# Kernel optimization log

Measured on AMD Instinct MI355X. Metric: run time of the kernel, lower is better.

The kernel has to match this reference:

```python
import jax, jax.numpy as jnp
import numpy as np

B, C, H, W = 8, 256, 56, 56
CI = 64  # inter_channels = C // reduction


def setup_inputs() -> dict:
    key = jax.random.key(0)
    ks = jax.random.split(key, 8)
    s = 0.05
    return {
        "x": jax.random.normal(ks[0], (B, C, H, W), jnp.float32),
        "Wq": jax.random.normal(ks[1], (CI, C), jnp.float32) * s,
        "bq": jax.random.normal(ks[2], (CI,), jnp.float32) * s,
        "Wk": jax.random.normal(ks[3], (CI, C), jnp.float32) * s,
        "bk": jax.random.normal(ks[4], (CI,), jnp.float32) * s,
        "Wv": jax.random.normal(ks[5], (C, C), jnp.float32) * s,
        "bv": jax.random.normal(ks[6], (C,), jnp.float32) * s,
        "gamma": jax.random.normal(ks[7], (1,), jnp.float32) * s,
    }


def reference(x, Wq, bq, Wk, bk, Wv, bv, gamma):
    b, c, h, w = x.shape
    n = h * w
    xf = x.reshape(b, c, n)  # [B, C, N]
    # 1x1 convs == per-pixel linear projections
    q = jnp.einsum('oc,bcn->bno', Wq, xf) + bq          # [B, N, CI]
    k = jnp.einsum('oc,bcn->bon', Wk, xf) + bk[:, None]  # [B, CI, N]
    score = jnp.einsum('bno,bom->bnm', q, k)             # [B, N, N] (no scaling, as in source)
    attention = jax.nn.softmax(score, axis=-1)
    v = jnp.einsum('oc,bcn->bon', Wv, xf) + bv[:, None]  # [B, C, N]
    # out[b,c,i] = sum_j v[b,c,j] * attention[b,i,j]  (== bmm(V, att^T))
    out = jnp.einsum('bcj,bij->bci', v, attention).reshape(b, c, h, w)
    return gamma[0] * out + x
```

## Files before the change

kernel.cpp:

```cpp
#include <hip/hip_runtime.h>


constexpr int B_  = 8;
constexpr int C_  = 256;
constexpr int CI_ = 64;
constexpr int N_  = 3136;
constexpr int JS  = 4;
constexpr int JT  = 32;
constexpr int VSP = 40;
constexpr int PN  = 64;
constexpr int XSP = C_ + 8;

typedef __attribute__((ext_vector_type(8))) short short8;
typedef __attribute__((ext_vector_type(4))) float f32x4;

static __device__ inline ushort f2b(float f) {
    unsigned u = __float_as_uint(f);
    return (ushort)((u + 0x7fffu + ((u >> 16) & 1u)) >> 16);
}
static __device__ inline float b2f(ushort h) {
    return __uint_as_float(((unsigned)h) << 16);
}

__global__ __launch_bounds__(256)
void pre_kernel(const float* __restrict__ x,
                const float* __restrict__ Wq, const float* __restrict__ Wk,
                const float* __restrict__ Wv,
                ushort* __restrict__ xT, ushort* __restrict__ wqk, ushort* __restrict__ wv)
{
    __shared__ float ts[64][65];
    const int bx  = blockIdx.x;
    const int tid = threadIdx.x;

    if (bx >= B_ * 196) {
        int i = (bx - B_ * 196) * 256 + tid;
        if (i < 16384)      wqk[i] = f2b(Wq[i]);
        else if (i < 32768) wqk[i] = f2b(Wk[i - 16384]);
        wv[i] = f2b(Wv[i]);
        return;
    }

    const int b  = bx / 196;
    const int rm = bx % 196;
    const int n0 = (rm >> 2) * 64;
    const int c0 = (rm & 3) * 64;

    const float* src = x + ((size_t)b * C_ + c0) * N_ + n0;
    #pragma unroll
    for (int rep = 0; rep < 16; rep++) {
        int e = rep * 256 + tid;
        int c = e >> 6, n = e & 63;
        ts[c][n] = src[(size_t)c * N_ + n];
    }
    __syncthreads();
    ushort* dst = xT + ((size_t)b * N_ + n0) * C_ + c0;
    #pragma unroll
    for (int rep = 0; rep < 8; rep++) {
        int e = rep * 256 + tid;
        int n = e >> 5, c2 = (e & 31) * 2;
        ushort2 o;
        o.x = f2b(ts[c2][n]);
        o.y = f2b(ts[c2 + 1][n]);
        *(ushort2*)(dst + (size_t)n * C_ + c2) = o;
    }
}

__global__ __launch_bounds__(256)
void proj_kernel(const ushort* __restrict__ xT, const ushort* __restrict__ wqk,
                 const ushort* __restrict__ wv,
                 const float* __restrict__ bq, const float* __restrict__ bk,
                 const float* __restrict__ bv,
                 ushort* __restrict__ qb, ushort* __restrict__ kb, ushort* __restrict__ vt)
{
    __shared__ ushort xs[PN][XSP];
    const int b   = blockIdx.x / 49;
    const int n0  = (blockIdx.x % 49) * PN;
    const int tid = threadIdx.x;
    const int w    = tid >> 6;
    const int lane = tid & 63;
    const int m16  = lane & 15;
    const int quad = lane >> 4;

    {
        const ushort* src = xT + ((size_t)b * N_ + n0) * C_;
        #pragma unroll
        for (int rep = 0; rep < 8; rep++) {
            int e = rep * 256 + tid;
            int row = e >> 5, ch = (e & 31) * 8;
            *(short8*)&xs[row][ch] = *(const short8*)(src + (size_t)row * C_ + ch);
        }
    }
    __syncthreads();

    {
        f32x4 acc[2][4];
        #pragma unroll
        for (int mt = 0; mt < 2; mt++)
            #pragma unroll
            for (int nt = 0; nt < 4; nt++) acc[mt][nt] = (f32x4){0.f, 0.f, 0.f, 0.f};

        #pragma unroll
        for (int kk = 0; kk < 8; kk++) {
            short8 af[2];
            #pragma unroll
            for (int mt = 0; mt < 2; mt++)
                af[mt] = *(const short8*)(wqk + (size_t)(w * 32 + mt * 16 + m16) * C_ + kk * 32 + quad * 8);
            #pragma unroll
            for (int nt = 0; nt < 4; nt++) {
                short8 bf = *(const short8*)&xs[nt * 16 + m16][kk * 32 + quad * 8];
                #pragma unroll
                for (int mt = 0; mt < 2; mt++)
                    acc[mt][nt] = __builtin_amdgcn_mfma_f32_16x16x32_bf16(af[mt], bf, acc[mt][nt], 0, 0, 0);
            }
        }
        const float* bias = (w < 2) ? bq : bk;
        ushort* dst = (w < 2) ? qb : kb;
        const int obase = (w & 1) * 32;
        #pragma unroll
        for (int mt = 0; mt < 2; mt++) {
            f32x4 bs = *(const f32x4*)(bias + obase + mt * 16 + quad * 4);
            #pragma unroll
            for (int nt = 0; nt < 4; nt++) {
                ushort4 pk;
                pk.x = f2b(acc[mt][nt][0] + bs[0]);
                pk.y = f2b(acc[mt][nt][1] + bs[1]);
                pk.z = f2b(acc[mt][nt][2] + bs[2]);
                pk.w = f2b(acc[mt][nt][3] + bs[3]);
                *(ushort4*)(dst + ((size_t)b * N_ + n0 + nt * 16 + m16) * CI_ + obase + mt * 16 + quad * 4) = pk;
            }
        }
    }

    {
        f32x4 vacc[4][4];
        #pragma unroll
        for (int mt = 0; mt < 4; mt++)
            #pragma unroll
            for (int nt = 0; nt < 4; nt++) vacc[mt][nt] = (f32x4){0.f, 0.f, 0.f, 0.f};

        #pragma unroll
        for (int kk = 0; kk < 8; kk++) {
            short8 af[4];
            #pragma unroll
            for (int mt = 0; mt < 4; mt++)
                af[mt] = *(const short8*)&xs[mt * 16 + m16][kk * 32 + quad * 8];
            #pragma unroll
            for (int nt = 0; nt < 4; nt++) {
                short8 bf = *(const short8*)(wv + (size_t)(w * 64 + nt * 16 + m16) * C_ + kk * 32 + quad * 8);
                #pragma unroll
                for (int mt = 0; mt < 4; mt++)
                    vacc[mt][nt] = __builtin_amdgcn_mfma_f32_16x16x32_bf16(af[mt], bf, vacc[mt][nt], 0, 0, 0);
            }
        }
        #pragma unroll
        for (int nt = 0; nt < 4; nt++) {
            int c = w * 64 + nt * 16 + m16;
            float bvc = bv[c];
            #pragma unroll
            for (int mt = 0; mt < 4; mt++) {
                ushort4 pk;
                pk.x = f2b(vacc[mt][nt][0] + bvc);
                pk.y = f2b(vacc[mt][nt][1] + bvc);
                pk.z = f2b(vacc[mt][nt][2] + bvc);
                pk.w = f2b(vacc[mt][nt][3] + bvc);
                *(ushort4*)(vt + ((size_t)b * C_ + c) * N_ + n0 + mt * 16 + quad * 4) = pk;
            }
        }
    }
}

__global__ __launch_bounds__(256, 5)
void attn_kernel(const ushort* __restrict__ qb, const ushort* __restrict__ kb,
                 const ushort* __restrict__ vt,
                 ushort* __restrict__ op, float* __restrict__ lp)
{
    __shared__ __align__(16) ushort vs[C_][VSP];

    const int bx   = blockIdx.x;
    const int js   = bx & (JS - 1);
    const int t    = (bx >> 2) % 98;
    const int b    = bx / (98 * JS);
    const int tid  = threadIdx.x;
    const int w    = tid >> 6;
    const int lane = tid & 63;
    const int m16  = lane & 15;
    const int quad = lane >> 4;
    const int i0   = t * 32 + (w & 1) * 16;
    const int ch0  = (w >> 1) * 128;

    const int steps = (js == 0) ? 13 : 12;
    const int jbase = ((js == 0) ? 0 : (1 + 12 * js)) * JT;

    const ushort* vtb = vt + (size_t)b * C_ * N_;
    const ushort* kbb = kb + (size_t)b * N_ * CI_;

    short8 qf[2];
    {
        const ushort* qbase = qb + ((size_t)b * N_ + i0 + m16) * CI_;
        qf[0] = *(const short8*)(qbase + quad * 8);
        qf[1] = *(const short8*)(qbase + 32 + quad * 8);
    }

    f32x4 O[8];
    #pragma unroll
    for (int ct = 0; ct < 8; ct++) O[ct] = (f32x4){0.f, 0.f, 0.f, 0.f};
    float lsum = 0.f;

    const int sc  = tid >> 2;
    const int seg = tid & 3;
    const int p0  = (seg & 1) * 16 + (seg >> 1) * 4;

    short8 pr[4];
    #define PREFETCH(J0)                                                       \
        {                                                                      \
            _Pragma("unroll")                                                  \
            for (int p = 0; p < 4; p++)                                        \
                pr[p] = *(const short8*)(vtb + (size_t)(p * 64 + sc) * N_ + (J0) + seg * 8); \
        }
    #define COMMIT()                                                           \
        {                                                                      \
            _Pragma("unroll")                                                  \
            for (int p = 0; p < 4; p++) {                                      \
                *(ushort4*)&vs[p * 64 + sc][p0]     = ((const ushort4*)&pr[p])[0]; \
                *(ushort4*)&vs[p * 64 + sc][p0 + 8] = ((const ushort4*)&pr[p])[1]; \
            }                                                                  \
        }

    PREFETCH(jbase)
    COMMIT()
    __syncthreads();

    for (int st = 0; st < steps; st++) {
        const int j0 = jbase + st * JT;
        if (st + 1 < steps) PREFETCH(j0 + JT)

        short8 pa;
        #pragma unroll
        for (int h = 0; h < 2; h++) {
            const ushort* krow = kbb + (size_t)(j0 + h * 16 + m16) * CI_;
            short8 kf0 = *(const short8*)(krow + quad * 8);
            short8 kf1 = *(const short8*)(krow + 32 + quad * 8);
            f32x4 T = (f32x4){0.f, 0.f, 0.f, 0.f};
            T = __builtin_amdgcn_mfma_f32_16x16x32_bf16(kf0, qf[0], T, 0, 0, 0);
            T = __builtin_amdgcn_mfma_f32_16x16x32_bf16(kf1, qf[1], T, 0, 0, 0);
            #pragma unroll
            for (int r = 0; r < 4; r++) {
                float pv = __expf(T[r] - 12.0f);
                lsum += pv;
                pa[h * 4 + r] = (short)f2b(pv);
            }
        }

        #pragma unroll
        for (int ct = 0; ct < 8; ct++) {
            short8 vf = *(const short8*)&vs[ch0 + ct * 16 + m16][quad * 8];
            O[ct] = __builtin_amdgcn_mfma_f32_16x16x32_bf16(pa, vf, O[ct], 0, 0, 0);
        }
        __syncthreads();
        if (st + 1 < steps) COMMIT()
        __syncthreads();
    }

    {
        float v = lsum;
        v += __shfl_xor(v, 16);
        v += __shfl_xor(v, 32);
        if (w < 2 && lane < 16)
            lp[(size_t)(b * JS + js) * N_ + i0 + lane] = v;
    }

    ushort* opb = op + (size_t)(b * JS + js) * C_ * N_;
    #pragma unroll
    for (int ct = 0; ct < 8; ct++) {
        ushort4 pk;
        pk.x = f2b(O[ct][0]);
        pk.y = f2b(O[ct][1]);
        pk.z = f2b(O[ct][2]);
        pk.w = f2b(O[ct][3]);
        *(ushort4*)(opb + (size_t)(ch0 + ct * 16 + m16) * N_ + i0 + quad * 4) = pk;
    }
    #undef PREFETCH
    #undef COMMIT
}

__global__ __launch_bounds__(256)
void reduce_kernel(const ushort* __restrict__ op, const float* __restrict__ lp,
                   const float* __restrict__ x, const float* __restrict__ gamma_p,
                   float* __restrict__ out)
{
    const int g  = blockIdx.x * 256 + threadIdx.x;
    const int i4 = g % (N_ / 4);
    const int c  = (g / (N_ / 4)) % C_;
    const int b  = g / ((N_ / 4) * C_);
    const size_t io = (size_t)i4 * 4;
    const float g0 = gamma_p[0];

    f32x4 acc = (f32x4){0.f, 0.f, 0.f, 0.f};
    f32x4 lt  = (f32x4){0.f, 0.f, 0.f, 0.f};
    #pragma unroll
    for (int js = 0; js < JS; js++) {
        ushort4 a = *(const ushort4*)(op + ((size_t)(b * JS + js) * C_ + c) * N_ + io);
        f32x4   l = *(const f32x4*)(lp + (size_t)(b * JS + js) * N_ + io);
        acc[0] += b2f(a.x); acc[1] += b2f(a.y); acc[2] += b2f(a.z); acc[3] += b2f(a.w);
        lt += l;
    }

    const size_t xo = ((size_t)b * C_ + c) * N_ + io;
    f32x4 xv = *(const f32x4*)(x + xo);
    f32x4 ov;
    #pragma unroll
    for (int u = 0; u < 4; u++) ov[u] = acc[u] * (g0 / lt[u]) + xv[u];
    *(f32x4*)(out + xo) = ov;
}

extern "C" void kernel_launch(void* const* d_in, const int* in_sizes, int n_in,
                              void* d_out, int out_size, void* d_ws, size_t ws_size,
                              hipStream_t stream)
{
    const float* x  = (const float*)d_in[0];
    const float* Wq = (const float*)d_in[1];
    const float* bq = (const float*)d_in[2];
    const float* Wk = (const float*)d_in[3];
    const float* bk = (const float*)d_in[4];
    const float* Wv = (const float*)d_in[5];
    const float* bv = (const float*)d_in[6];
    const float* gm = (const float*)d_in[7];
    float* out = (float*)d_out;

    ushort* qb   = (ushort*)d_ws;
    ushort* kb   = qb + (size_t)B_ * N_ * CI_;
    ushort* vt   = kb + (size_t)B_ * N_ * CI_;
    ushort* xT   = vt + (size_t)B_ * C_ * N_;
    ushort* wqk  = xT + (size_t)B_ * N_ * C_;
    ushort* wv   = wqk + 128 * C_;
    ushort* op   = wv + 256 * C_;
    float*  lpf  = (float*)(op + (size_t)B_ * JS * C_ * N_);

    hipLaunchKernelGGL(pre_kernel, dim3(B_ * 196 + 256), dim3(256), 0, stream,
                       x, Wq, Wk, Wv, xT, wqk, wv);
    hipLaunchKernelGGL(proj_kernel, dim3(B_ * 49), dim3(256), 0, stream,
                       xT, wqk, wv, bq, bk, bv, qb, kb, vt);
    hipLaunchKernelGGL(attn_kernel, dim3(B_ * 98 * JS), dim3(256), 0, stream,
                       qb, kb, vt, op, lpf);
    hipLaunchKernelGGL(reduce_kernel, dim3(B_ * C_ * (N_ / 4) / 256), dim3(256), 0, stream,
                       op, lpf, x, gm, out);
}
```

Before: 234.8 us.

## Double query rows per attention wave, double-buffer V tile, prefetch K, halve proj tile

Each attention wave now handles two 16-row query groups, so every K fragment and V tile in shared memory serves twice as many MFMAs. The grid is halved and each split covers about 25 key steps. The V staging tile is double-buffered, which removes one barrier per step, and K fragments are prefetched into registers one step ahead. The projection kernel tile drops from 64 to 32 pixels to double its block count. The cost is higher register use, with launch bounds lowered to 3 waves, and twice the LDS per block.

```diff
diff --git a/kernel.cpp b/kernel.cpp
--- a/kernel.cpp
+++ b/kernel.cpp
@@ -8,7 +8,7 @@
 constexpr int JS  = 4;
 constexpr int JT  = 32;
 constexpr int VSP = 40;
-constexpr int PN  = 64;
+constexpr int PN  = 32;
 constexpr int XSP = C_ + 8;
 
 typedef __attribute__((ext_vector_type(8))) short short8;
@@ -73,8 +73,8 @@
                  ushort* __restrict__ qb, ushort* __restrict__ kb, ushort* __restrict__ vt)
 {
     __shared__ ushort xs[PN][XSP];
-    const int b   = blockIdx.x / 49;
-    const int n0  = (blockIdx.x % 49) * PN;
+    const int b   = blockIdx.x / 98;
+    const int n0  = (blockIdx.x % 98) * PN;
     const int tid = threadIdx.x;
     const int w    = tid >> 6;
     const int lane = tid & 63;
@@ -84,7 +84,7 @@
     {
         const ushort* src = xT + ((size_t)b * N_ + n0) * C_;
         #pragma unroll
-        for (int rep = 0; rep < 8; rep++) {
+        for (int rep = 0; rep < 4; rep++) {
             int e = rep * 256 + tid;
             int row = e >> 5, ch = (e & 31) * 8;
             *(short8*)&xs[row][ch] = *(const short8*)(src + (size_t)row * C_ + ch);
@@ -93,11 +93,11 @@
     __syncthreads();
 
     {
-        f32x4 acc[2][4];
+        f32x4 acc[2][2];
         #pragma unroll
         for (int mt = 0; mt < 2; mt++)
             #pragma unroll
-            for (int nt = 0; nt < 4; nt++) acc[mt][nt] = (f32x4){0.f, 0.f, 0.f, 0.f};
+            for (int nt = 0; nt < 2; nt++) acc[mt][nt] = (f32x4){0.f, 0.f, 0.f, 0.f};
 
         #pragma unroll
         for (int kk = 0; kk < 8; kk++) {
@@ -106,7 +106,7 @@
             for (int mt = 0; mt < 2; mt++)
                 af[mt] = *(const short8*)(wqk + (size_t)(w * 32 + mt * 16 + m16) * C_ + kk * 32 + quad * 8);
             #pragma unroll
-            for (int nt = 0; nt < 4; nt++) {
+            for (int nt = 0; nt < 2; nt++) {
                 short8 bf = *(const short8*)&xs[nt * 16 + m16][kk * 32 + quad * 8];
                 #pragma unroll
                 for (int mt = 0; mt < 2; mt++)
@@ -120,7 +120,7 @@
         for (int mt = 0; mt < 2; mt++) {
             f32x4 bs = *(const f32x4*)(bias + obase + mt * 16 + quad * 4);
             #pragma unroll
-            for (int nt = 0; nt < 4; nt++) {
+            for (int nt = 0; nt < 2; nt++) {
                 ushort4 pk;
                 pk.x = f2b(acc[mt][nt][0] + bs[0]);
                 pk.y = f2b(acc[mt][nt][1] + bs[1]);
@@ -132,23 +132,23 @@
     }
 
     {
-        f32x4 vacc[4][4];
-        #pragma unroll
-        for (int mt = 0; mt < 4; mt++)
+        f32x4 vacc[2][4];
+        #pragma unroll
+        for (int mt = 0; mt < 2; mt++)
             #pragma unroll
             for (int nt = 0; nt < 4; nt++) vacc[mt][nt] = (f32x4){0.f, 0.f, 0.f, 0.f};
 
         #pragma unroll
         for (int kk = 0; kk < 8; kk++) {
-            short8 af[4];
-            #pragma unroll
-            for (int mt = 0; mt < 4; mt++)
+            short8 af[2];
+            #pragma unroll
+            for (int mt = 0; mt < 2; mt++)
                 af[mt] = *(const short8*)&xs[mt * 16 + m16][kk * 32 + quad * 8];
             #pragma unroll
             for (int nt = 0; nt < 4; nt++) {
                 short8 bf = *(const short8*)(wv + (size_t)(w * 64 + nt * 16 + m16) * C_ + kk * 32 + quad * 8);
                 #pragma unroll
-                for (int mt = 0; mt < 4; mt++)
+                for (int mt = 0; mt < 2; mt++)
                     vacc[mt][nt] = __builtin_amdgcn_mfma_f32_16x16x32_bf16(af[mt], bf, vacc[mt][nt], 0, 0, 0);
             }
         }
@@ -157,7 +157,7 @@
             int c = w * 64 + nt * 16 + m16;
             float bvc = bv[c];
             #pragma unroll
-            for (int mt = 0; mt < 4; mt++) {
+            for (int mt = 0; mt < 2; mt++) {
                 ushort4 pk;
                 pk.x = f2b(vacc[mt][nt][0] + bvc);
                 pk.y = f2b(vacc[mt][nt][1] + bvc);
@@ -169,118 +169,152 @@
     }
 }
 
-__global__ __launch_bounds__(256, 5)
+__global__ __launch_bounds__(256, 3)
 void attn_kernel(const ushort* __restrict__ qb, const ushort* __restrict__ kb,
                  const ushort* __restrict__ vt,
                  ushort* __restrict__ op, float* __restrict__ lp)
 {
-    __shared__ __align__(16) ushort vs[C_][VSP];
+    __shared__ __align__(16) ushort vs[2][C_][VSP];
 
     const int bx   = blockIdx.x;
     const int js   = bx & (JS - 1);
-    const int t    = (bx >> 2) % 98;
-    const int b    = bx / (98 * JS);
+    const int t    = (bx >> 2) % 49;
+    const int b    = bx / (49 * JS);
     const int tid  = threadIdx.x;
     const int w    = tid >> 6;
     const int lane = tid & 63;
     const int m16  = lane & 15;
     const int quad = lane >> 4;
-    const int i0   = t * 32 + (w & 1) * 16;
+    const int i0   = t * 64 + (w & 1) * 32;
     const int ch0  = (w >> 1) * 128;
 
-    const int steps = (js == 0) ? 13 : 12;
-    const int jbase = ((js == 0) ? 0 : (1 + 12 * js)) * JT;
+    const int steps = (js < 2) ? 25 : 24;
+    const int jbase = ((js < 2) ? js * 25 : 50 + (js - 2) * 24) * JT;
 
     const ushort* vtb = vt + (size_t)b * C_ * N_;
     const ushort* kbb = kb + (size_t)b * N_ * CI_;
 
-    short8 qf[2];
-    {
-        const ushort* qbase = qb + ((size_t)b * N_ + i0 + m16) * CI_;
-        qf[0] = *(const short8*)(qbase + quad * 8);
-        qf[1] = *(const short8*)(qbase + 32 + quad * 8);
-    }
-
-    f32x4 O[8];
-    #pragma unroll
-    for (int ct = 0; ct < 8; ct++) O[ct] = (f32x4){0.f, 0.f, 0.f, 0.f};
-    float lsum = 0.f;
-
-    const int sc  = tid >> 2;
-    const int seg = tid & 3;
-    const int p0  = (seg & 1) * 16 + (seg >> 1) * 4;
-
-    short8 pr[4];
-    #define PREFETCH(J0)                                                       \
-        {                                                                      \
-            _Pragma("unroll")                                                  \
-            for (int p = 0; p < 4; p++)                                        \
-                pr[p] = *(const short8*)(vtb + (size_t)(p * 64 + sc) * N_ + (J0) + seg * 8); \
-        }
-    #define COMMIT()                                                           \
-        {                                                                      \
-            _Pragma("unroll")                                                  \
-            for (int p = 0; p < 4; p++) {                                      \
-                *(ushort4*)&vs[p * 64 + sc][p0]     = ((const ushort4*)&pr[p])[0]; \
-                *(ushort4*)&vs[p * 64 + sc][p0 + 8] = ((const ushort4*)&pr[p])[1]; \
-            }                                                                  \
-        }
-
-    PREFETCH(jbase)
-    COMMIT()
+    short8 qf[2][2];
+    #pragma unroll
+    for (int qg = 0; qg < 2; qg++) {
+        const ushort* qbase = qb + ((size_t)b * N_ + i0 + qg * 16 + m16) * CI_;
+        qf[qg][0] = *(const short8*)(qbase + quad * 8);
+        qf[qg][1] = *(const short8*)(qbase + 32 + quad * 8);
+    }
+
+    f32x4 O[2][8];
+    #pragma unroll
+    for (int qg = 0; qg < 2; qg++)
+        #pragma unroll
+        for (int ct = 0; ct < 8; ct++) O[qg][ct] = (f32x4){0.f, 0.f, 0.f, 0.f};
+    float lsum[2] = {0.f, 0.f};
+
+    const int sc = tid >> 2;
+    const int s4 = (tid & 3) * 4;
+    const int sp = (tid & 3) * 8;
+
+    uint2 vr[4][2];
+    #define VLOAD(J0)                                                           \
+        {                                                                       \
+            _Pragma("unroll")                                                   \
+            for (int p = 0; p < 4; p++) {                                       \
+                const ushort* r = vtb + (size_t)(p * 64 + sc) * N_ + (J0);      \
+                vr[p][0] = *(const uint2*)(r + s4);                             \
+                vr[p][1] = *(const uint2*)(r + 16 + s4);                        \
+            }                                                                   \
+        }
+    #define VCOMMIT(BUF)                                                        \
+        {                                                                       \
+            _Pragma("unroll")                                                   \
+            for (int p = 0; p < 4; p++) {                                       \
+                uint4 t4;                                                       \
+                t4.x = vr[p][0].x; t4.y = vr[p][0].y;                           \
+                t4.z = vr[p][1].x; t4.w = vr[p][1].y;                           \
+                *(uint4*)&vs[BUF][p * 64 + sc][sp] = t4;                        \
+            }                                                                   \
+        }
+    #define KLOAD(DST, J0)                                                      \
+        {                                                                       \
+            _Pragma("unroll")                                                   \
+            for (int h = 0; h < 2; h++) {                                       \
+                const ushort* kr = kbb + (size_t)((J0) + h * 16 + m16) * CI_;   \
+                DST[h * 2 + 0] = *(const short8*)(kr + quad * 8);               \
+                DST[h * 2 + 1] = *(const short8*)(kr + 32 + quad * 8);          \
+            }                                                                   \
+        }
+
+    short8 kc[4];
+    KLOAD(kc, jbase)
+    VLOAD(jbase)
+    VCOMMIT(0)
     __syncthreads();
 
+    int buf = 0;
     for (int st = 0; st < steps; st++) {
         const int j0 = jbase + st * JT;
-        if (st + 1 < steps) PREFETCH(j0 + JT)
-
-        short8 pa;
+        const bool more = (st + 1 < steps);
+        short8 kn[4];
+        if (more) { VLOAD(j0 + JT) KLOAD(kn, j0 + JT) }
+
+        short8 pa[2];
         #pragma unroll
         for (int h = 0; h < 2; h++) {
-            const ushort* krow = kbb + (size_t)(j0 + h * 16 + m16) * CI_;
-            short8 kf0 = *(const short8*)(krow + quad * 8);
-            short8 kf1 = *(const short8*)(krow + 32 + quad * 8);
-            f32x4 T = (f32x4){0.f, 0.f, 0.f, 0.f};
-            T = __builtin_amdgcn_mfma_f32_16x16x32_bf16(kf0, qf[0], T, 0, 0, 0);
-            T = __builtin_amdgcn_mfma_f32_16x16x32_bf16(kf1, qf[1], T, 0, 0, 0);
+            f32x4 T0 = (f32x4){0.f, 0.f, 0.f, 0.f};
+            f32x4 T1 = (f32x4){0.f, 0.f, 0.f, 0.f};
+            T0 = __builtin_amdgcn_mfma_f32_16x16x32_bf16(kc[h * 2 + 0], qf[0][0], T0, 0, 0, 0);
+            T1 = __builtin_amdgcn_mfma_f32_16x16x32_bf16(kc[h * 2 + 0], qf[1][0], T1, 0, 0, 0);
+            T0 = __builtin_amdgcn_mfma_f32_16x16x32_bf16(kc[h * 2 + 1], qf[0][1], T0, 0, 0, 0);
+            T1 = __builtin_amdgcn_mfma_f32_16x16x32_bf16(kc[h * 2 + 1], qf[1][1], T1, 0, 0, 0);
             #pragma unroll
             for (int r = 0; r < 4; r++) {
-                float pv = __expf(T[r] - 12.0f);
-                lsum += pv;
-                pa[h * 4 + r] = (short)f2b(pv);
+                float p0 = __expf(T0[r] - 12.0f);
+                float p1 = __expf(T1[r] - 12.0f);
+                lsum[0] += p0;
+                lsum[1] += p1;
+                pa[0][h * 4 + r] = (short)f2b(p0);
+                pa[1][h * 4 + r] = (short)f2b(p1);
             }
         }
 
         #pragma unroll
         for (int ct = 0; ct < 8; ct++) {
-            short8 vf = *(const short8*)&vs[ch0 + ct * 16 + m16][quad * 8];
-            O[ct] = __builtin_amdgcn_mfma_f32_16x16x32_bf16(pa, vf, O[ct], 0, 0, 0);
-        }
+            short8 vf = *(const short8*)&vs[buf][ch0 + ct * 16 + m16][quad * 8];
+            O[0][ct] = __builtin_amdgcn_mfma_f32_16x16x32_bf16(pa[0], vf, O[0][ct], 0, 0, 0);
+            O[1][ct] = __builtin_amdgcn_mfma_f32_16x16x32_bf16(pa[1], vf, O[1][ct], 0, 0, 0);
+        }
+
+        if (more) VCOMMIT(buf ^ 1)
         __syncthreads();
-        if (st + 1 < steps) COMMIT()
-        __syncthreads();
-    }
-
-    {
-        float v = lsum;
+        if (more) {
+            kc[0] = kn[0]; kc[1] = kn[1]; kc[2] = kn[2]; kc[3] = kn[3];
+        }
+        buf ^= 1;
+    }
+    #undef VLOAD
+    #undef VCOMMIT
+    #undef KLOAD
+
+    #pragma unroll
+    for (int qg = 0; qg < 2; qg++) {
+        float v = lsum[qg];
         v += __shfl_xor(v, 16);
         v += __shfl_xor(v, 32);
-        if (w < 2 && lane < 16)
-            lp[(size_t)(b * JS + js) * N_ + i0 + lane] = v;
+        if ((w >> 1) == 0 && lane < 16)
+            lp[(size_t)(b * JS + js) * N_ + i0 + qg * 16 + lane] = v;
     }
 
     ushort* opb = op + (size_t)(b * JS + js) * C_ * N_;
     #pragma unroll
-    for (int ct = 0; ct < 8; ct++) {
-        ushort4 pk;
-        pk.x = f2b(O[ct][0]);
-        pk.y = f2b(O[ct][1]);
-        pk.z = f2b(O[ct][2]);
-        pk.w = f2b(O[ct][3]);
-        *(ushort4*)(opb + (size_t)(ch0 + ct * 16 + m16) * N_ + i0 + quad * 4) = pk;
-    }
-    #undef PREFETCH
-    #undef COMMIT
+    for (int qg = 0; qg < 2; qg++)
+        #pragma unroll
+        for (int ct = 0; ct < 8; ct++) {
+            ushort4 pk;
+            pk.x = f2b(O[qg][ct][0]);
+            pk.y = f2b(O[qg][ct][1]);
+            pk.z = f2b(O[qg][ct][2]);
+            pk.w = f2b(O[qg][ct][3]);
+            *(ushort4*)(opb + (size_t)(ch0 + ct * 16 + m16) * N_ + i0 + qg * 16 + quad * 4) = pk;
+        }
 }
 
 __global__ __launch_bounds__(256)
@@ -338,9 +372,9 @@
 
     hipLaunchKernelGGL(pre_kernel, dim3(B_ * 196 + 256), dim3(256), 0, stream,
                        x, Wq, Wk, Wv, xT, wqk, wv);
-    hipLaunchKernelGGL(proj_kernel, dim3(B_ * 49), dim3(256), 0, stream,
+    hipLaunchKernelGGL(proj_kernel, dim3(B_ * 98), dim3(256), 0, stream,
                        xT, wqk, wv, bq, bk, bv, qb, kb, vt);
-    hipLaunchKernelGGL(attn_kernel, dim3(B_ * 98 * JS), dim3(256), 0, stream,
+    hipLaunchKernelGGL(attn_kernel, dim3(B_ * 49 * JS), dim3(256), 0, stream,
                        qb, kb, vt, op, lpf);
     hipLaunchKernelGGL(reduce_kernel, dim3(B_ * C_ * (N_ / 4) / 256), dim3(256), 0, stream,
                        op, lpf, x, gm, out);
```

New measurement: 270.6 us. +15.2%, slower.
